# Kernel optimization log

Measured on AMD Instinct MI355X. Metric: run time of the kernel, lower is better.

Reference implementation:

```python
import jax, jax.numpy as jnp
import numpy as np

K = 5          # retrieval_k
EPS = 1e-8     # torch cosine_similarity eps


def setup_inputs() -> dict:
    key = jax.random.key(0)
    ks = jax.random.split(key, 10)
    B, M, D, H = 1024, 65536, 384, 384
    return {
        "query": jax.random.normal(ks[0], (B, D), jnp.float32),
        "mem_vectors": jax.random.normal(ks[1], (M, D), jnp.float32),
        "coords": jax.random.normal(ks[2], (M, 2), jnp.float32),
        "spatial_weights": jax.random.normal(ks[3], (H, 2), jnp.float32),
        "W_ih": jax.random.normal(ks[4], (H, D), jnp.float32) * 0.05,
        "b_ih": jax.random.normal(ks[5], (H,), jnp.float32) * 0.05,
        "W_hh": jax.random.normal(ks[6], (H, H), jnp.float32) * 0.05,
        "b_hh": jax.random.normal(ks[7], (H,), jnp.float32) * 0.05,
        "W_g": jax.random.normal(ks[8], (H, D), jnp.float32) * 0.05,
        "b_g": jax.random.normal(ks[9], (H,), jnp.float32) * 0.05,
    }


def reference(query, mem_vectors, coords, spatial_weights,
              W_ih, b_ih, W_hh, b_hh, W_g, b_g):
    # --- spatial_activation: 1/(1+dist) from coords to mean of spatial_weights ---
    center = spatial_weights.mean(axis=0)                      # [2]
    dists = jnp.linalg.norm(coords - center, axis=1)           # [M]
    activations = 1.0 / (1.0 + dists)                          # [M]

    # --- retrieve_memories: cosine similarity + spatial activation, top-k ---
    qn = jnp.linalg.norm(query, axis=1, keepdims=True)         # [B,1]
    mn = jnp.linalg.norm(mem_vectors, axis=1, keepdims=True)   # [M,1]
    dots = query @ mem_vectors.T                               # [B,M]
    sim = dots / jnp.maximum(qn * mn.T, EPS)                   # cosine w/ torch eps
    total_sim = sim + activations[None, :]                     # [B,M]
    _, topk_idx = jax.lax.top_k(total_sim, K)                  # [B,K]
    retrieved = mem_vectors[topk_idx]                          # [B,K,D]

    # --- contextualize: tiny RNN over [query, retrieved...] then gated mix ---
    seq = jnp.concatenate([query[:, None, :], retrieved], axis=1)  # [B,K+1,D]
    x_proj = jnp.einsum('btd,hd->bth', seq, W_ih) + b_ih           # [B,K+1,H]

    def step(h, x_t):  # x_t: [B,H]
        h = jnp.tanh(x_t + h @ W_hh.T + b_hh)
        return h, None

    h0 = jnp.zeros((query.shape[0], W_hh.shape[0]), query.dtype)
    h, _ = jax.lax.scan(step, h0, jnp.swapaxes(x_proj, 0, 1))      # [B,H]

    gate = jax.nn.sigmoid(query @ W_g.T + b_g)                     # [B,H]
    direct = query @ W_ih.T + b_ih                                 # [B,H]
    return gate * h + (1.0 - gate) * direct
```

## Files before the change

kernel.cpp:

```cpp
#include <hip/hip_runtime.h>
#include <math.h>

namespace {

typedef float f32x4 __attribute__((ext_vector_type(4)));
typedef float f32x16 __attribute__((ext_vector_type(16)));
typedef short bf16x8 __attribute__((ext_vector_type(8)));
typedef unsigned short ushort_t;

constexpr int B  = 1024;
constexpr int M  = 65536;
constexpr int D  = 384;
constexpr int H  = 384;
constexpr int KK = 5;
constexpr int NC = 128;
constexpr int CHUNK = M / NC;
constexpr float FEPS = 1e-8f;

__device__ __forceinline__ ushort_t f2bf(float x) {
  unsigned int u = __float_as_uint(x);
  unsigned int r = (u + 0x7FFFu + ((u >> 16) & 1u)) >> 16;
  return (ushort_t)r;
}
__device__ __forceinline__ float bf2f(ushort_t h) {
  return __uint_as_float(((unsigned int)h) << 16);
}

__device__ __forceinline__ void async16(const ushort_t* g, ushort_t* l) {
  __builtin_amdgcn_global_load_lds(
      (const __attribute__((address_space(1))) unsigned int*)g,
      (__attribute__((address_space(3))) unsigned int*)l, 16, 0, 0);
}

__device__ __forceinline__ void insert3b(unsigned int* k, unsigned int v) {
  unsigned int t0 = min(k[0], v); k[0] = max(k[0], v);
  unsigned int t1 = min(k[1], t0); k[1] = max(k[1], t0);
  k[2] = max(k[2], t1);
}
__device__ __forceinline__ void insert5b(unsigned int* k, unsigned int v) {
  unsigned int t0 = min(k[0], v); k[0] = max(k[0], v);
  unsigned int t1 = min(k[1], t0); k[1] = max(k[1], t0);
  unsigned int t2 = min(k[2], t1); k[2] = max(k[2], t1);
  unsigned int t3 = min(k[3], t2); k[3] = max(k[3], t2);
  k[4] = max(k[4], t3);
}

__device__ __forceinline__ int swz_koff(int lane) {
  return (((lane & 3) ^ ((lane >> 3) & 3)) * 8);
}

__global__ __launch_bounds__(256) void k_prep(
    const float* __restrict__ q, const float* __restrict__ mem,
    const float* __restrict__ coords, const float* __restrict__ sw,
    const float* __restrict__ W_ih, const float* __restrict__ W_hh,
    const float* __restrict__ W_g,
    ushort_t* __restrict__ qh, ushort_t* __restrict__ mh,
    float2* __restrict__ f2a, float2* __restrict__ f2b,
    ushort_t* __restrict__ wihh, ushort_t* __restrict__ wihl,
    ushort_t* __restrict__ whhh, ushort_t* __restrict__ whhl,
    ushort_t* __restrict__ wgh, ushort_t* __restrict__ wgl) {
  int wv = threadIdx.x >> 6, lane = threadIdx.x & 63;
  int bid = blockIdx.x;
  if (bid < M/4) {
    int r = bid*4 + wv;
    float cx = 0.f, cy = 0.f;
    for (int i = lane; i < H; i += 64) { cx += sw[2*i]; cy += sw[2*i+1]; }
#pragma unroll
    for (int o = 32; o > 0; o >>= 1) { cx += __shfl_xor(cx, o); cy += __shfl_xor(cy, o); }
    cx *= (1.0f/384.0f); cy *= (1.0f/384.0f);
    float2 x[3]; float s = 0.f;
#pragma unroll
    for (int k = 0; k < 3; ++k) {
      x[k] = ((const float2*)(mem + (size_t)r*D))[lane + 64*k];
      s += x[k].x*x[k].x + x[k].y*x[k].y;
    }
#pragma unroll
    for (int o = 32; o > 0; o >>= 1) s += __shfl_xor(s, o);
#pragma unroll
    for (int k = 0; k < 3; ++k) {
      ushort2 hh; hh.x = f2bf(x[k].x); hh.y = f2bf(x[k].y);
      ((ushort2*)(mh + (size_t)r*D))[lane + 64*k] = hh;
    }
    if (lane == 0) {
      float mn = sqrtf(s);
      float dx = coords[2*r] - cx, dy = coords[2*r+1] - cy;
      float act = 1.0f / (1.0f + sqrtf(dx*dx + dy*dy));
      f2a[r] = make_float2(1.0f / mn, act + 2.0f);
      f2b[r] = make_float2(mn, act);
    }
  } else if (bid < M/4 + B/4) {
    int r = (bid - M/4)*4 + wv;
    float2 x[3]; float s = 0.f;
#pragma unroll
    for (int k = 0; k < 3; ++k) {
      x[k] = ((const float2*)(q + (size_t)r*D))[lane + 64*k];
      s += x[k].x*x[k].x + x[k].y*x[k].y;
    }
#pragma unroll
    for (int o = 32; o > 0; o >>= 1) s += __shfl_xor(s, o);
    float inv = 1.0f / sqrtf(s);
#pragma unroll
    for (int k = 0; k < 3; ++k) {
      ushort2 nn; nn.x = f2bf(x[k].x * inv); nn.y = f2bf(x[k].y * inv);
      ((ushort2*)(qh + (size_t)r*D))[lane + 64*k] = nn;
    }
  } else {
    int r = (bid - M/4 - B/4)*4 + wv;
    const float* src; ushort_t* dh; ushort_t* dl;
    if (r < 384)      { src = W_ih + (size_t)r*D;       dh = wihh + (size_t)r*D;       dl = wihl + (size_t)r*D; }
    else if (r < 768) { src = W_hh + (size_t)(r-384)*D; dh = whhh + (size_t)(r-384)*D; dl = whhl + (size_t)(r-384)*D; }
    else              { src = W_g  + (size_t)(r-768)*D; dh = wgh  + (size_t)(r-768)*D; dl = wgl  + (size_t)(r-768)*D; }
#pragma unroll
    for (int k = 0; k < 3; ++k) {
      float2 v = ((const float2*)src)[lane + 64*k];
      ushort_t h0 = f2bf(v.x), h1 = f2bf(v.y);
      ushort2 hh; hh.x = h0; hh.y = h1;
      ushort2 ll; ll.x = f2bf(v.x - bf2f(h0)); ll.y = f2bf(v.y - bf2f(h1));
      ((ushort2*)dh)[lane + 64*k] = hh;
      ((ushort2*)dl)[lane + 64*k] = ll;
    }
  }
}

__global__ __launch_bounds__(256, 2) void k_sim(
    const ushort_t* __restrict__ qh,
    const ushort_t* __restrict__ mh,
    const float2* __restrict__ f2a, unsigned int* __restrict__ keybuf) {
  __shared__ __align__(16) ushort_t sQh[2*8192];
  __shared__ __align__(16) ushort_t sMh[2*8192];
  __shared__ __align__(16) float2 sF[CHUNK];

  const int tid = threadIdx.x, lane = tid & 63, wave = tid >> 6;
  const int wr = wave >> 1, wc = wave & 1;
  const int l31 = lane & 31, half = lane >> 5;
  const int flat = blockIdx.x;
  const int k8 = flat & 7, qb = (flat >> 3) & 7, mgrp = flat >> 6;
  const int nc = (mgrp << 3) | k8;
  const int rowoff = lane >> 2, koff = swz_koff(lane);
  const int gsw = (l31 >> 1) & 3;
  const size_t qrow0 = (size_t)qb * 128;

  ((float4*)sF)[tid] = ((const float4*)(f2a + (size_t)nc * CHUNK))[tid];

  auto stage = [&](int buf, int mt, int k6) {
    const size_t mrow0 = (size_t)nc * CHUNK + (size_t)mt * 128;
    const int kt = k6 * 64;
#pragma unroll
    for (int n = 0; n < 8; ++n) {
      int f = wave*8 + n;
      int arr = f >> 4, sub = f & 15, kb = sub >> 3, slot = sub & 7;
      const ushort_t* src = arr == 0 ? qh : mh;
      ushort_t* dst = (arr == 0 ? sQh : sMh) + buf*8192;
      size_t rowb = arr == 0 ? qrow0 : mrow0;
      async16(src + (rowb + slot*16 + rowoff)*D + kt + kb*32 + koff,
              dst + kb*4096 + slot*512 + lane*8);
    }
  };

  unsigned int keys[2][3];
#pragma unroll
  for (int j = 0; j < 2; ++j) { keys[j][0] = 0; keys[j][1] = 0; keys[j][2] = 0; }

  stage(0, 0, 0);
  __syncthreads();

  int cur = 0;
  f32x16 acc[2][2];

  for (int mt = 0; mt < 4; ++mt) {
#pragma unroll
    for (int i = 0; i < 2; ++i)
#pragma unroll
      for (int j = 0; j < 2; ++j) acc[i][j] = (f32x16)0.0f;

#pragma unroll
    for (int k6 = 0; k6 < 6; ++k6) {
      const int nmt = (k6 == 5) ? mt + 1 : mt;
      const int nk6 = (k6 == 5) ? 0 : k6 + 1;
      if (nmt < 4) stage(cur ^ 1, nmt, nk6);

      const int bufo = cur * 8192;
#pragma unroll
      for (int kb = 0; kb < 2; ++kb) {
        const int base = bufo + kb*4096;
        bf16x8 ah[2][2], bh[2][2];
#pragma unroll
        for (int i = 0; i < 2; ++i)
#pragma unroll
          for (int s = 0; s < 2; ++s) {
            int gra = ((s*2 + half) ^ gsw) * 8;
            int ro = base + (wr*64 + i*32 + l31)*32 + gra;
            ah[i][s] = *(const bf16x8*)&sMh[ro];
            int co = base + (wc*64 + i*32 + l31)*32 + gra;
            bh[i][s] = *(const bf16x8*)&sQh[co];
          }
#pragma unroll
        for (int i = 0; i < 2; ++i)
#pragma unroll
          for (int j = 0; j < 2; ++j)
#pragma unroll
            for (int s = 0; s < 2; ++s)
              acc[i][j] = __builtin_amdgcn_mfma_f32_32x32x16_bf16(ah[i][s], bh[j][s], acc[i][j], 0, 0, 0);
      }

      if (k6 == 5) {
#pragma unroll
        for (int i = 0; i < 2; ++i)
#pragma unroll
          for (int rg = 0; rg < 4; ++rg)
#pragma unroll
            for (int rr = 0; rr < 4; ++rr) {
              int rl = wr*64 + i*32 + half*4 + rr + 8*rg;
              float2 fa = sF[mt*128 + rl];
              unsigned int idx = (unsigned int)(((nc & 1) << 9) | (mt*128 + rl));
              float v0 = fmaf(acc[i][0][rg*4+rr], fa.x, fa.y);
              insert3b(keys[0], (__float_as_uint(v0) & 0xFFFFFC00u) | idx);
              float v1 = fmaf(acc[i][1][rg*4+rr], fa.x, fa.y);
              insert3b(keys[1], (__float_as_uint(v1) & 0xFFFFFC00u) | idx);
            }
      }

      __syncthreads();
      cur ^= 1;
    }
  }

#pragma unroll
  for (int j = 0; j < 2; ++j) {
    int q_local = wc*64 + j*32 + l31;
    int c = wr*2 + half;
    size_t off = ((size_t)(qb*128 + q_local) * NC + nc) * 12 + c*3;
    keybuf[off+0] = keys[j][0];
    keybuf[off+1] = keys[j][1];
    keybuf[off+2] = keys[j][2];
  }
}

__global__ __launch_bounds__(256) void k_merge(
    const unsigned int* __restrict__ keybuf,
    const float* __restrict__ query, const float* __restrict__ memv,
    const float2* __restrict__ f2b,
    ushort_t* __restrict__ xsh, ushort_t* __restrict__ xsl) {
  __shared__ int sCand[16];
  __shared__ float sSimv[16];
  __shared__ int sTop[KK];
  const int tid = threadIdx.x, lane = tid & 63, wave = tid >> 6;
  const int q = blockIdx.x;

  if (wave == 0) {
    const unsigned int* kb = keybuf + (size_t)q * (NC*12) + (size_t)lane * 24;
    unsigned int k5[5] = {0,0,0,0,0};
#pragma unroll
    for (int c = 0; c < 6; ++c) {
      uint4 v = *(const uint4*)(kb + c*4);
      insert5b(k5, v.x); insert5b(k5, v.y); insert5b(k5, v.z); insert5b(k5, v.w);
    }
#pragma unroll
    for (int p = 0; p < 16; ++p) {
      unsigned int bk = k5[0]; int blv = lane;
#pragma unroll
      for (int off = 1; off < 64; off <<= 1) {
        unsigned int ok = (unsigned int)__shfl_xor((int)bk, off);
        int ol = __shfl_xor(blv, off);
        if (ok > bk || (ok == bk && ol < blv)) { bk = ok; blv = ol; }
      }
      if (lane == blv) { k5[0]=k5[1]; k5[1]=k5[2]; k5[2]=k5[3]; k5[3]=k5[4]; k5[4]=0; }
      if (lane == 0) sCand[p] = (blv << 10) | (int)(bk & 1023u);
    }
  }
  __syncthreads();

  float qv[6]; float sq = 0.f;
#pragma unroll
  for (int k = 0; k < 6; ++k) { qv[k] = query[(size_t)q*D + lane + 64*k]; sq += qv[k]*qv[k]; }
#pragma unroll
  for (int o = 32; o > 0; o >>= 1) sq += __shfl_xor(sq, o);
  float qn = sqrtf(sq);

#pragma unroll
  for (int pp = 0; pp < 4; ++pp) {
    int p = wave*4 + pp;
    int mi = sCand[p];
    float d = 0.f;
#pragma unroll
    for (int k = 0; k < 6; ++k) d += qv[k] * memv[(size_t)mi*D + lane + 64*k];
#pragma unroll
    for (int o = 32; o > 0; o >>= 1) d += __shfl_xor(d, o);
    if (lane == 0) {
      float2 fb = f2b[mi];
      sSimv[p] = d / fmaxf(qn * fb.x, FEPS) + fb.y;
    }
  }
  __syncthreads();

  if (tid == 0) {
    float cv[16]; int ci[16];
#pragma unroll
    for (int p = 0; p < 16; ++p) { cv[p] = sSimv[p]; ci[p] = sCand[p]; }
    for (int s = 0; s < KK; ++s) {
      int best = -1; float bv = -1e30f; int bi = 0x7FFFFFFF;
      for (int p = 0; p < 16; ++p) {
        if (ci[p] < 0) continue;
        if (cv[p] > bv || (cv[p] == bv && ci[p] < bi)) { best = p; bv = cv[p]; bi = ci[p]; }
      }
      sTop[s] = ci[best];
      ci[best] = -1;
    }
  }
  __syncthreads();

#pragma unroll
  for (int rep = 0; rep < 2; ++rep) {
    int t = wave + rep*4;
    if (t < 6) {
      const float* src = (t == 0) ? (query + (size_t)q*D)
                                  : (memv + (size_t)sTop[t-1]*D);
      size_t g = (size_t)q*6 + t;
#pragma unroll
      for (int k = 0; k < 3; ++k) {
        float2 v = ((const float2*)src)[lane + 64*k];
        ushort_t h0 = f2bf(v.x), h1 = f2bf(v.y);
        ushort2 hh; hh.x = h0; hh.y = h1;
        ushort2 ll; ll.x = f2bf(v.x - bf2f(h0)); ll.y = f2bf(v.y - bf2f(h1));
        ((ushort2*)(xsh + g*D))[lane + 64*k] = hh;
        ((ushort2*)(xsl + g*D))[lane + 64*k] = ll;
      }
    }
  }
}

__global__ __launch_bounds__(256) void k_tail1(
    const ushort_t* __restrict__ xsh, const ushort_t* __restrict__ xsl,
    const ushort_t* __restrict__ wihh, const ushort_t* __restrict__ wihl,
    const ushort_t* __restrict__ wgh, const ushort_t* __restrict__ wgl,
    const float* __restrict__ b_ih, const float* __restrict__ b_hh,
    const float* __restrict__ b_g,
    float* __restrict__ xp, float* __restrict__ gate,
    ushort_t* __restrict__ hoh, ushort_t* __restrict__ hol) {
  __shared__ __align__(16) ushort_t sAh[64*128];
  __shared__ __align__(16) ushort_t sAl[64*128];
  __shared__ __align__(16) ushort_t sWh[64*128];
  __shared__ __align__(16) ushort_t sWl[64*128];

  const int tid = threadIdx.x, lane = tid & 63, wave = tid >> 6;
  const int wr = wave >> 1, wc = wave & 1;
  const int t = lane & 15, quad = lane >> 4;
  const bool xmode = blockIdx.x < 96;
  const int cbase = blockIdx.y * 64;
  const int rowoff = lane >> 2, koff = swz_koff(lane);
  const int pq = (quad ^ ((t >> 1) & 3)) * 8;

  const ushort_t* gp[4];
  if (wave < 2) {
    const ushort_t* base = (wave == 0) ? xsh : xsl;
#pragma unroll
    for (int slot = 0; slot < 4; ++slot) {
      int rl = slot*16 + rowoff;
      size_t row = xmode ? (size_t)(blockIdx.x*64 + rl)
                         : (size_t)((blockIdx.x - 96)*64 + rl) * 6;
      gp[slot] = base + row*D + koff;
    }
  } else {
#pragma unroll
    for (int slot = 0; slot < 4; ++slot) {
      int rl = slot*16 + rowoff;
      const ushort_t* wsrc = xmode ? (wave == 2 ? wihh : wihl)
                                   : (wave == 2 ? wgh  : wgl);
      gp[slot] = wsrc + (size_t)(cbase + rl) * D + koff;
    }
  }
  ushort_t* ldst = (wave == 0) ? sAh : (wave == 1) ? sAl : (wave == 2) ? sWh : sWl;

  f32x4 acc[2][2];
#pragma unroll
  for (int i = 0; i < 2; ++i)
#pragma unroll
    for (int j = 0; j < 2; ++j) acc[i][j] = (f32x4)0.0f;

  for (int r3 = 0; r3 < 3; ++r3) {
    __syncthreads();
#pragma unroll
    for (int s = 0; s < 4; ++s)
#pragma unroll
      for (int slot = 0; slot < 4; ++slot)
        async16(gp[slot] + r3*128 + s*32, ldst + s*2048 + slot*512 + lane*8);
    __syncthreads();
#pragma unroll
    for (int s = 0; s < 4; ++s) {
      bf16x8 ah[2], al[2], bh[2], bl[2];
#pragma unroll
      for (int i = 0; i < 2; ++i) {
        int ro = s*2048 + (wr*32 + i*16 + t)*32 + pq;
        ah[i] = *(const bf16x8*)&sAh[ro];
        al[i] = *(const bf16x8*)&sAl[ro];
        int co = s*2048 + (wc*32 + i*16 + t)*32 + pq;
        bh[i] = *(const bf16x8*)&sWh[co];
        bl[i] = *(const bf16x8*)&sWl[co];
      }
#pragma unroll
      for (int i = 0; i < 2; ++i)
#pragma unroll
        for (int j = 0; j < 2; ++j) {
          acc[i][j] = __builtin_amdgcn_mfma_f32_16x16x32_bf16(ah[i], bh[j], acc[i][j], 0, 0, 0);
          acc[i][j] = __builtin_amdgcn_mfma_f32_16x16x32_bf16(ah[i], bl[j], acc[i][j], 0, 0, 0);
          acc[i][j] = __builtin_amdgcn_mfma_f32_16x16x32_bf16(al[i], bh[j], acc[i][j], 0, 0, 0);
        }
    }
  }

#pragma unroll
  for (int i = 0; i < 2; ++i)
#pragma unroll
    for (int j = 0; j < 2; ++j)
#pragma unroll
      for (int r = 0; r < 4; ++r) {
        int rloc = wr*32 + i*16 + quad*4 + r;
        int h = cbase + wc*32 + j*16 + t;
        float a = acc[i][j][r];
        if (xmode) {
          int g = blockIdx.x*64 + rloc;
          float v = a + b_ih[h];
          xp[(size_t)g*H + h] = v;
          int b = g / 6;
          if (g - b*6 == 0) {
            float hv = tanhf(v + b_hh[h]);
            ushort_t hi = f2bf(hv);
            hoh[(size_t)b*H + h] = hi;
            hol[(size_t)b*H + h] = f2bf(hv - bf2f(hi));
          }
        } else {
          int rq = (blockIdx.x - 96)*64 + rloc;
          gate[(size_t)rq*H + h] = 1.0f / (1.0f + expf(-(a + b_g[h])));
        }
      }
}

template<int LAST>
__global__ __launch_bounds__(256) void k_rnn(
    const ushort_t* __restrict__ hih, const ushort_t* __restrict__ hil,
    const ushort_t* __restrict__ whhh, const ushort_t* __restrict__ whhl,
    const float* __restrict__ b_hh, const float* __restrict__ xp,
    const float* __restrict__ gate, int step,
    ushort_t* __restrict__ hoh, ushort_t* __restrict__ hol,
    float* __restrict__ out) {
  __shared__ __align__(16) ushort_t sAh[64*128];
  __shared__ __align__(16) ushort_t sAl[64*128];
  __shared__ __align__(16) ushort_t sWh[64*128];
  __shared__ __align__(16) ushort_t sWl[64*128];

  const int tid = threadIdx.x, lane = tid & 63, wave = tid >> 6;
  const int wr = wave >> 1, wc = wave & 1;
  const int t = lane & 15, quad = lane >> 4;
  const int rbase = blockIdx.x * 64, cbase = blockIdx.y * 64;
  const int rowoff = lane >> 2, koff = swz_koff(lane);
  const int pq = (quad ^ ((t >> 1) & 3)) * 8;

  const ushort_t* gp[4];
#pragma unroll
  for (int slot = 0; slot < 4; ++slot) {
    int rl = slot*16 + rowoff;
    const ushort_t* src =
        (wave == 0) ? hih + (size_t)(rbase + rl)*D :
        (wave == 1) ? hil + (size_t)(rbase + rl)*D :
        (wave == 2) ? whhh + (size_t)(cbase + rl)*D :
                      whhl + (size_t)(cbase + rl)*D;
    gp[slot] = src + koff;
  }
  ushort_t* ldst = (wave == 0) ? sAh : (wave == 1) ? sAl : (wave == 2) ? sWh : sWl;

  f32x4 acc[2][2];
#pragma unroll
  for (int i = 0; i < 2; ++i)
#pragma unroll
    for (int j = 0; j < 2; ++j) acc[i][j] = (f32x4)0.0f;

  for (int r3 = 0; r3 < 3; ++r3) {
    __syncthreads();
#pragma unroll
    for (int s = 0; s < 4; ++s)
#pragma unroll
      for (int slot = 0; slot < 4; ++slot)
        async16(gp[slot] + r3*128 + s*32, ldst + s*2048 + slot*512 + lane*8);
    __syncthreads();
#pragma unroll
    for (int s = 0; s < 4; ++s) {
      bf16x8 ah[2], al[2], bh[2], bl[2];
#pragma unroll
      for (int i = 0; i < 2; ++i) {
        int ro = s*2048 + (wr*32 + i*16 + t)*32 + pq;
        ah[i] = *(const bf16x8*)&sAh[ro];
        al[i] = *(const bf16x8*)&sAl[ro];
        int co = s*2048 + (wc*32 + i*16 + t)*32 + pq;
        bh[i] = *(const bf16x8*)&sWh[co];
        bl[i] = *(const bf16x8*)&sWl[co];
      }
#pragma unroll
      for (int i = 0; i < 2; ++i)
#pragma unroll
        for (int j = 0; j < 2; ++j) {
          acc[i][j] = __builtin_amdgcn_mfma_f32_16x16x32_bf16(ah[i], bh[j], acc[i][j], 0, 0, 0);
          acc[i][j] = __builtin_amdgcn_mfma_f32_16x16x32_bf16(ah[i], bl[j], acc[i][j], 0, 0, 0);
          acc[i][j] = __builtin_amdgcn_mfma_f32_16x16x32_bf16(al[i], bh[j], acc[i][j], 0, 0, 0);
        }
    }
  }

#pragma unroll
  for (int i = 0; i < 2; ++i)
#pragma unroll
    for (int j = 0; j < 2; ++j)
#pragma unroll
      for (int r = 0; r < 4; ++r) {
        int row = rbase + wr*32 + i*16 + quad*4 + r;
        int h = cbase + wc*32 + j*16 + t;
        float v = acc[i][j][r] + b_hh[h] + xp[(size_t)row*(6*H) + step*H + h];
        float hv = tanhf(v);
        if (LAST) {
          float g = gate[(size_t)row*H + h];
          out[(size_t)row*H + h] = g*hv + (1.0f - g)*xp[(size_t)row*(6*H) + h];
        } else {
          ushort_t hi = f2bf(hv);
          hoh[(size_t)row*H + h] = hi;
          hol[(size_t)row*H + h] = f2bf(hv - bf2f(hi));
        }
      }
}

}

extern "C" void kernel_launch(void* const* d_in, const int* in_sizes, int n_in,
                              void* d_out, int out_size, void* d_ws, size_t ws_size,
                              hipStream_t stream) {
  const float* query = (const float*)d_in[0];
  const float* memv  = (const float*)d_in[1];
  const float* coords= (const float*)d_in[2];
  const float* sw    = (const float*)d_in[3];
  const float* W_ih  = (const float*)d_in[4];
  const float* b_ih  = (const float*)d_in[5];
  const float* W_hh  = (const float*)d_in[6];
  const float* b_hh  = (const float*)d_in[7];
  const float* W_g   = (const float*)d_in[8];
  const float* b_g   = (const float*)d_in[9];
  float* out = (float*)d_out;

  char* p = (char*)d_ws;
  auto alloc = [&](size_t bytes) {
    char* r = p; p += (bytes + 255) & ~(size_t)255; return r;
  };
  ushort_t* qh  = (ushort_t*)alloc((size_t)B * D * 2);
  ushort_t* mh  = (ushort_t*)alloc((size_t)M * D * 2);
  float2* f2a   = (float2*)alloc((size_t)M * 8);
  float2* f2b   = (float2*)alloc((size_t)M * 8);
  ushort_t* wihh = (ushort_t*)alloc((size_t)H * D * 2);
  ushort_t* wihl = (ushort_t*)alloc((size_t)H * D * 2);
  ushort_t* whhh = (ushort_t*)alloc((size_t)H * D * 2);
  ushort_t* whhl = (ushort_t*)alloc((size_t)H * D * 2);
  ushort_t* wgh  = (ushort_t*)alloc((size_t)H * D * 2);
  ushort_t* wgl  = (ushort_t*)alloc((size_t)H * D * 2);
  unsigned int* keybuf = (unsigned int*)alloc((size_t)B * NC * 12 * 4);
  ushort_t* xsh = (ushort_t*)alloc((size_t)B * 6 * D * 2);
  ushort_t* xsl = (ushort_t*)alloc((size_t)B * 6 * D * 2);
  float* xp     = (float*)alloc((size_t)B * 6 * H * 4);
  float* gate   = (float*)alloc((size_t)B * H * 4);
  ushort_t* hAh = (ushort_t*)alloc((size_t)B * H * 2);
  ushort_t* hAl = (ushort_t*)alloc((size_t)B * H * 2);
  ushort_t* hBh = (ushort_t*)alloc((size_t)B * H * 2);
  ushort_t* hBl = (ushort_t*)alloc((size_t)B * H * 2);

  k_prep<<<M/4 + B/4 + 288, 256, 0, stream>>>(
      query, memv, coords, sw, W_ih, W_hh, W_g,
      qh, mh, f2a, f2b,
      wihh, wihl, whhh, whhl, wgh, wgl);
  k_sim<<<1024, 256, 0, stream>>>(qh, mh, f2a, keybuf);
  k_merge<<<B, 256, 0, stream>>>(keybuf, query, memv, f2b, xsh, xsl);
  k_tail1<<<dim3(112, 6), 256, 0, stream>>>(
      xsh, xsl, wihh, wihl, wgh, wgl,
      b_ih, b_hh, b_g, xp, gate, hAh, hAl);
  k_rnn<0><<<dim3(16, 6), 256, 0, stream>>>(hAh, hAl, whhh, whhl, b_hh, xp, gate, 1, hBh, hBl, out);
  k_rnn<0><<<dim3(16, 6), 256, 0, stream>>>(hBh, hBl, whhh, whhl, b_hh, xp, gate, 2, hAh, hAl, out);
  k_rnn<0><<<dim3(16, 6), 256, 0, stream>>>(hAh, hAl, whhh, whhl, b_hh, xp, gate, 3, hBh, hBl, out);
  k_rnn<0><<<dim3(16, 6), 256, 0, stream>>>(hBh, hBl, whhh, whhl, b_hh, xp, gate, 4, hAh, hAl, out);
  k_rnn<1><<<dim3(16, 6), 256, 0, stream>>>(hAh, hAl, whhh, whhl, b_hh, xp, gate, 5, hBh, hBl, out);
}
```

Measured before the change: 340.5 us.

## Fuse five RNN step launches into one persistent kernel with grid barrier

New measurement: 403.8 us. +18.6%, slower.

```diff
diff --git a/kernel.cpp b/kernel.cpp
--- a/kernel.cpp
+++ b/kernel.cpp
@@ -47,6 +47,19 @@
 
 __device__ __forceinline__ int swz_koff(int lane) {
   return (((lane & 3) ^ ((lane >> 3) & 3)) * 8);
+}
+
+__device__ __forceinline__ void grid_barrier(unsigned int* bar, unsigned int target) {
+  __threadfence();
+  __syncthreads();
+  if (threadIdx.x == 0) {
+    __hip_atomic_fetch_add(bar, 1u, __ATOMIC_ACQ_REL, __HIP_MEMORY_SCOPE_AGENT);
+    while (__hip_atomic_load(bar, __ATOMIC_ACQUIRE, __HIP_MEMORY_SCOPE_AGENT) < target) {
+      __builtin_amdgcn_s_sleep(8);
+    }
+  }
+  __syncthreads();
+  __threadfence();
 }
 
 __global__ __launch_bounds__(256) void k_prep(
@@ -58,9 +71,11 @@
     float2* __restrict__ f2a, float2* __restrict__ f2b,
     ushort_t* __restrict__ wihh, ushort_t* __restrict__ wihl,
     ushort_t* __restrict__ whhh, ushort_t* __restrict__ whhl,
-    ushort_t* __restrict__ wgh, ushort_t* __restrict__ wgl) {
+    ushort_t* __restrict__ wgh, ushort_t* __restrict__ wgl,
+    unsigned int* __restrict__ bar) {
   int wv = threadIdx.x >> 6, lane = threadIdx.x & 63;
   int bid = blockIdx.x;
+  if (bid == 0 && threadIdx.x == 0) *bar = 0u;
   if (bid < M/4) {
     int r = bid*4 + wv;
     float cx = 0.f, cy = 0.f;
@@ -435,14 +450,13 @@
       }
 }
 
-template<int LAST>
-__global__ __launch_bounds__(256) void k_rnn(
-    const ushort_t* __restrict__ hih, const ushort_t* __restrict__ hil,
+__global__ __launch_bounds__(256) void k_rnn_all(
+    ushort_t* __restrict__ hAh, ushort_t* __restrict__ hAl,
+    ushort_t* __restrict__ hBh, ushort_t* __restrict__ hBl,
     const ushort_t* __restrict__ whhh, const ushort_t* __restrict__ whhl,
     const float* __restrict__ b_hh, const float* __restrict__ xp,
-    const float* __restrict__ gate, int step,
-    ushort_t* __restrict__ hoh, ushort_t* __restrict__ hol,
-    float* __restrict__ out) {
+    const float* __restrict__ gate,
+    float* __restrict__ out, unsigned int* __restrict__ bar) {
   __shared__ __align__(16) ushort_t sAh[64*128];
   __shared__ __align__(16) ushort_t sAl[64*128];
   __shared__ __align__(16) ushort_t sWh[64*128];
@@ -454,76 +468,89 @@
   const int rbase = blockIdx.x * 64, cbase = blockIdx.y * 64;
   const int rowoff = lane >> 2, koff = swz_koff(lane);
   const int pq = (quad ^ ((t >> 1) & 3)) * 8;
-
-  const ushort_t* gp[4];
+  const unsigned int nblk = gridDim.x * gridDim.y;
+
+  const ushort_t* gpw[4];
 #pragma unroll
   for (int slot = 0; slot < 4; ++slot) {
     int rl = slot*16 + rowoff;
-    const ushort_t* src =
-        (wave == 0) ? hih + (size_t)(rbase + rl)*D :
-        (wave == 1) ? hil + (size_t)(rbase + rl)*D :
-        (wave == 2) ? whhh + (size_t)(cbase + rl)*D :
-                      whhl + (size_t)(cbase + rl)*D;
-    gp[slot] = src + koff;
+    gpw[slot] = ((wave == 2) ? whhh : whhl) + (size_t)(cbase + rl)*D + koff;
   }
   ushort_t* ldst = (wave == 0) ? sAh : (wave == 1) ? sAl : (wave == 2) ? sWh : sWl;
 
-  f32x4 acc[2][2];
-#pragma unroll
-  for (int i = 0; i < 2; ++i)
-#pragma unroll
-    for (int j = 0; j < 2; ++j) acc[i][j] = (f32x4)0.0f;
-
-  for (int r3 = 0; r3 < 3; ++r3) {
-    __syncthreads();
-#pragma unroll
-    for (int s = 0; s < 4; ++s)
-#pragma unroll
-      for (int slot = 0; slot < 4; ++slot)
-        async16(gp[slot] + r3*128 + s*32, ldst + s*2048 + slot*512 + lane*8);
-    __syncthreads();
-#pragma unroll
-    for (int s = 0; s < 4; ++s) {
-      bf16x8 ah[2], al[2], bh[2], bl[2];
-#pragma unroll
-      for (int i = 0; i < 2; ++i) {
-        int ro = s*2048 + (wr*32 + i*16 + t)*32 + pq;
-        ah[i] = *(const bf16x8*)&sAh[ro];
-        al[i] = *(const bf16x8*)&sAl[ro];
-        int co = s*2048 + (wc*32 + i*16 + t)*32 + pq;
-        bh[i] = *(const bf16x8*)&sWh[co];
-        bl[i] = *(const bf16x8*)&sWl[co];
-      }
-#pragma unroll
-      for (int i = 0; i < 2; ++i)
-#pragma unroll
-        for (int j = 0; j < 2; ++j) {
-          acc[i][j] = __builtin_amdgcn_mfma_f32_16x16x32_bf16(ah[i], bh[j], acc[i][j], 0, 0, 0);
-          acc[i][j] = __builtin_amdgcn_mfma_f32_16x16x32_bf16(ah[i], bl[j], acc[i][j], 0, 0, 0);
-          acc[i][j] = __builtin_amdgcn_mfma_f32_16x16x32_bf16(al[i], bh[j], acc[i][j], 0, 0, 0);
+  for (int s = 1; s <= 5; ++s) {
+    const ushort_t* ih = (s & 1) ? hAh : hBh;
+    const ushort_t* il = (s & 1) ? hAl : hBl;
+    ushort_t* oh = (s & 1) ? hBh : hAh;
+    ushort_t* ol = (s & 1) ? hBl : hAl;
+
+    const ushort_t* gp[4];
+#pragma unroll
+    for (int slot = 0; slot < 4; ++slot) {
+      int rl = slot*16 + rowoff;
+      gp[slot] = (wave >= 2) ? gpw[slot]
+               : ((wave == 0) ? ih : il) + (size_t)(rbase + rl)*D + koff;
+    }
+
+    f32x4 acc[2][2];
+#pragma unroll
+    for (int i = 0; i < 2; ++i)
+#pragma unroll
+      for (int j = 0; j < 2; ++j) acc[i][j] = (f32x4)0.0f;
+
+    for (int r3 = 0; r3 < 3; ++r3) {
+      __syncthreads();
+#pragma unroll
+      for (int ss = 0; ss < 4; ++ss)
+#pragma unroll
+        for (int slot = 0; slot < 4; ++slot)
+          async16(gp[slot] + r3*128 + ss*32, ldst + ss*2048 + slot*512 + lane*8);
+      __syncthreads();
+#pragma unroll
+      for (int ss = 0; ss < 4; ++ss) {
+        bf16x8 ah[2], al[2], bh[2], bl[2];
+#pragma unroll
+        for (int i = 0; i < 2; ++i) {
+          int ro = ss*2048 + (wr*32 + i*16 + t)*32 + pq;
+          ah[i] = *(const bf16x8*)&sAh[ro];
+          al[i] = *(const bf16x8*)&sAl[ro];
+          int co = ss*2048 + (wc*32 + i*16 + t)*32 + pq;
+          bh[i] = *(const bf16x8*)&sWh[co];
+          bl[i] = *(const bf16x8*)&sWl[co];
         }
-    }
-  }
-
-#pragma unroll
-  for (int i = 0; i < 2; ++i)
-#pragma unroll
-    for (int j = 0; j < 2; ++j)
-#pragma unroll
-      for (int r = 0; r < 4; ++r) {
-        int row = rbase + wr*32 + i*16 + quad*4 + r;
-        int h = cbase + wc*32 + j*16 + t;
-        float v = acc[i][j][r] + b_hh[h] + xp[(size_t)row*(6*H) + step*H + h];
-        float hv = tanhf(v);
-        if (LAST) {
-          float g = gate[(size_t)row*H + h];
-          out[(size_t)row*H + h] = g*hv + (1.0f - g)*xp[(size_t)row*(6*H) + h];
-        } else {
-          ushort_t hi = f2bf(hv);
-          hoh[(size_t)row*H + h] = hi;
-          hol[(size_t)row*H + h] = f2bf(hv - bf2f(hi));
+#pragma unroll
+        for (int i = 0; i < 2; ++i)
+#pragma unroll
+          for (int j = 0; j < 2; ++j) {
+            acc[i][j] = __builtin_amdgcn_mfma_f32_16x16x32_bf16(ah[i], bh[j], acc[i][j], 0, 0, 0);
+            acc[i][j] = __builtin_amdgcn_mfma_f32_16x16x32_bf16(ah[i], bl[j], acc[i][j], 0, 0, 0);
+            acc[i][j] = __builtin_amdgcn_mfma_f32_16x16x32_bf16(al[i], bh[j], acc[i][j], 0, 0, 0);
+          }
+      }
+    }
+
+#pragma unroll
+    for (int i = 0; i < 2; ++i)
+#pragma unroll
+      for (int j = 0; j < 2; ++j)
+#pragma unroll
+        for (int r = 0; r < 4; ++r) {
+          int row = rbase + wr*32 + i*16 + quad*4 + r;
+          int h = cbase + wc*32 + j*16 + t;
+          float v = acc[i][j][r] + b_hh[h] + xp[(size_t)row*(6*H) + s*H + h];
+          float hv = tanhf(v);
+          if (s == 5) {
+            float g = gate[(size_t)row*H + h];
+            out[(size_t)row*H + h] = g*hv + (1.0f - g)*xp[(size_t)row*(6*H) + h];
+          } else {
+            ushort_t hi = f2bf(hv);
+            oh[(size_t)row*H + h] = hi;
+            ol[(size_t)row*H + h] = f2bf(hv - bf2f(hi));
+          }
         }
-      }
+
+    if (s < 5) grid_barrier(bar, nblk * (unsigned)s);
+  }
 }
 
 }
@@ -566,19 +593,17 @@
   ushort_t* hAl = (ushort_t*)alloc((size_t)B * H * 2);
   ushort_t* hBh = (ushort_t*)alloc((size_t)B * H * 2);
   ushort_t* hBl = (ushort_t*)alloc((size_t)B * H * 2);
+  unsigned int* bar = (unsigned int*)alloc(256);
 
   k_prep<<<M/4 + B/4 + 288, 256, 0, stream>>>(
       query, memv, coords, sw, W_ih, W_hh, W_g,
       qh, mh, f2a, f2b,
-      wihh, wihl, whhh, whhl, wgh, wgl);
+      wihh, wihl, whhh, whhl, wgh, wgl, bar);
   k_sim<<<1024, 256, 0, stream>>>(qh, mh, f2a, keybuf);
   k_merge<<<B, 256, 0, stream>>>(keybuf, query, memv, f2b, xsh, xsl);
   k_tail1<<<dim3(112, 6), 256, 0, stream>>>(
       xsh, xsl, wihh, wihl, wgh, wgl,
       b_ih, b_hh, b_g, xp, gate, hAh, hAl);
-  k_rnn<0><<<dim3(16, 6), 256, 0, stream>>>(hAh, hAl, whhh, whhl, b_hh, xp, gate, 1, hBh, hBl, out);
-  k_rnn<0><<<dim3(16, 6), 256, 0, stream>>>(hBh, hBl, whhh, whhl, b_hh, xp, gate, 2, hAh, hAl, out);
-  k_rnn<0><<<dim3(16, 6), 256, 0, stream>>>(hAh, hAl, whhh, whhl, b_hh, xp, gate, 3, hBh, hBl, out);
-  k_rnn<0><<<dim3(16, 6), 256, 0, stream>>>(hBh, hBl, whhh, whhl, b_hh, xp, gate, 4, hAh, hAl, out);
-  k_rnn<1><<<dim3(16, 6), 256, 0, stream>>>(hAh, hAl, whhh, whhl, b_hh, xp, gate, 5, hBh, hBl, out);
-}
+  k_rnn_all<<<dim3(16, 6), 256, 0, stream>>>(
+      hAh, hAl, hBh, hBl, whhh, whhl, b_hh, xp, gate, out, bar);
+}
```
